# Kernel tuning notes

Hardware: AMD Instinct MI355X
Metric: run time of the kernel (lower is better)

The kernel has to match this reference:

```python
import jax, jax.numpy as jnp
import numpy as np

N_NODES = 100000
N_EDGES = 3200000
IN_F = 128
HEADS = 8
OUT_C = 2  # GATConv out_channels hardcoded to 2 in the source
NEG_SLOPE = 0.2  # PyG GATConv default leaky_relu slope


def setup_inputs() -> dict:
    key = jax.random.key(0)
    ks = jax.random.split(key, 9)
    x = jax.random.normal(ks[0], (N_NODES, IN_F), dtype=jnp.float32)
    edge_index = jax.random.randint(ks[1], (2, N_EDGES), 0, N_NODES, dtype=jnp.int64)
    edge_attr = jax.random.uniform(ks[2], (N_EDGES, 1), dtype=jnp.float32)
    s = 1.0 / np.sqrt(IN_F)
    W = jax.random.normal(ks[3], (IN_F, HEADS * OUT_C), dtype=jnp.float32) * s
    att_src = jax.random.normal(ks[4], (HEADS, OUT_C), dtype=jnp.float32) * 0.5
    att_dst = jax.random.normal(ks[5], (HEADS, OUT_C), dtype=jnp.float32) * 0.5
    bias_gat = jnp.zeros((HEADS * OUT_C,), dtype=jnp.float32)
    W_fc = jax.random.normal(ks[6], (HEADS * OUT_C, 2), dtype=jnp.float32) * 0.25
    b_fc = jnp.zeros((2,), dtype=jnp.float32)
    return {"x": x, "edge_index": edge_index, "edge_attr": edge_attr,
            "W": W, "att_src": att_src, "att_dst": att_dst,
            "bias_gat": bias_gat, "W_fc": W_fc, "b_fc": b_fc}


def reference(x, edge_index, edge_attr, W, att_src, att_dst, bias_gat, W_fc, b_fc):
    # edge_attr is ignored: GATConv was built without edge_dim, matching the source.
    N = x.shape[0]
    # PyG GATConv adds self-loops by default
    loops = jnp.arange(N, dtype=edge_index.dtype)
    src = jnp.concatenate([edge_index[0], loops])  # [E']
    dst = jnp.concatenate([edge_index[1], loops])  # [E']

    h = (x @ W).reshape(N, HEADS, OUT_C)                 # [N,H,C]
    a_src = jnp.einsum('nhc,hc->nh', h, att_src)          # [N,H]
    a_dst = jnp.einsum('nhc,hc->nh', h, att_dst)          # [N,H]

    logits = jax.nn.leaky_relu(a_src[src] + a_dst[dst], negative_slope=NEG_SLOPE)  # [E',H]
    # segment softmax over edges grouped by destination node (self-loops ensure non-empty segments)
    seg_max = jax.ops.segment_max(logits, dst, num_segments=N)   # [N,H]
    p = jnp.exp(logits - seg_max[dst])                            # [E',H]
    seg_sum = jax.ops.segment_sum(p, dst, num_segments=N)         # [N,H]
    alpha = p / seg_sum[dst]                                      # [E',H]

    msg = alpha[:, :, None] * h[src]                              # [E',H,C]
    agg = jax.ops.segment_sum(msg, dst, num_segments=N)           # [N,H,C]
    gat_out = agg.reshape(N, HEADS * OUT_C) + bias_gat            # concat heads + bias
    return gat_out @ W_fc + b_fc                                  # [N,2]
```

## Files before the change

kernel.cpp:

```cpp
#include <hip/hip_runtime.h>
#include <hip/hip_fp16.h>

#define N_NODES 100000
#define IN_F 128
#define NF 16
#define HEADS 8
#define NEG_SLOPE 0.2f
#define LOG2E 1.44269504f

#define RB 128
#define LOG_RB 7
#define NB 782
#define SBITS 17
#define SMASK ((1u << SBITS) - 1)
#define BIN_C 4096
#define CAPB 4672


__device__ __forceinline__ void phase1_body(
    int pb, const float* __restrict__ x, const float* __restrict__ W,
    __half* __restrict__ rec, float* Ws)
{
    int t = threadIdx.x;
    for (int i = t; i < IN_F * NF; i += 512) Ws[i] = W[i];
    __syncthreads();

    int tid  = pb * 512 + t;
    int node = tid >> 4;
    int j    = tid & 15;
    if (node >= N_NODES) return;

    const float4* xr4 = (const float4*)(x + (size_t)node * IN_F);
    float acc = 0.f;
    #pragma unroll 8
    for (int k4 = 0; k4 < IN_F / 4; ++k4) {
        float4 xv = xr4[k4];
        acc = fmaf(xv.x, Ws[(4 * k4 + 0) * NF + j], acc);
        acc = fmaf(xv.y, Ws[(4 * k4 + 1) * NF + j], acc);
        acc = fmaf(xv.z, Ws[(4 * k4 + 2) * NF + j], acc);
        acc = fmaf(xv.w, Ws[(4 * k4 + 3) * NF + j], acc);
    }
    rec[(size_t)node * NF + j] = __float2half(acc);
}

__global__ __launch_bounds__(512) void fused_p1_bin(
    const int* __restrict__ ei, int* __restrict__ bin_cursor,
    unsigned* __restrict__ bins,
    const float* __restrict__ x, const float* __restrict__ W,
    __half* __restrict__ rec, int E, int SB)
{
    __shared__ union {
        struct {
            unsigned staging[BIN_C];
            unsigned short bin16[BIN_C];
            int hist[NB], offs[NB], cur[NB], gbase[NB];
            int wsum[8], woff[8];
        } b;
        float Ws[IN_F * NF];
    } sm;

    int idx = blockIdx.x;
    bool is_bin = (idx % 5 == 0) && (idx / 5 < SB);
    if (!is_bin) {
        int cb = (idx + 4) / 5; if (cb > SB) cb = SB;
        phase1_body(idx - cb, x, W, rec, sm.Ws);
        return;
    }

    int t = threadIdx.x;
    int base = (idx / 5) * BIN_C;
    int n_valid = E - base;
    if (n_valid > BIN_C) n_valid = BIN_C;
    if (n_valid < 0) n_valid = 0;

    int es[8], ed[8];
    #pragma unroll
    for (int k = 0; k < 8; ++k) {
        int i = t + 512 * k;
        bool v = i < n_valid;
        es[k] = v ? ei[base + i] : 0;
        ed[k] = v ? ei[E + base + i] : -1;
    }

    for (int b = t; b < NB; b += 512) sm.b.hist[b] = 0;
    __syncthreads();

    #pragma unroll
    for (int k = 0; k < 8; ++k)
        if (ed[k] >= 0) atomicAdd(&sm.b.hist[ed[k] >> LOG_RB], 1);
    __syncthreads();

    int h2[2], sum = 0;
    #pragma unroll
    for (int k = 0; k < 2; ++k) {
        int b = 2 * t + k;
        h2[k] = (b < NB) ? sm.b.hist[b] : 0;
        sum += h2[k];
    }
    int lane = t & 63, wid = t >> 6;
    int v = sum;
    #pragma unroll
    for (int o = 1; o < 64; o <<= 1) {
        int u = __shfl_up(v, o);
        if (lane >= o) v += u;
    }
    if (lane == 63) sm.b.wsum[wid] = v;
    __syncthreads();
    if (t == 0) { int r = 0; for (int w = 0; w < 8; ++w) { sm.b.woff[w] = r; r += sm.b.wsum[w]; } }
    __syncthreads();
    int run = sm.b.woff[wid] + v - sum;
    #pragma unroll
    for (int k = 0; k < 2; ++k) {
        int b = 2 * t + k;
        if (b < NB) { sm.b.offs[b] = run; sm.b.cur[b] = run; }
        run += h2[k];
    }
    __syncthreads();
    for (int b = t; b < NB; b += 512)
        sm.b.gbase[b] = sm.b.hist[b] ? atomicAdd(&bin_cursor[b], sm.b.hist[b]) : 0;
    __syncthreads();

    #pragma unroll
    for (int k = 0; k < 8; ++k) {
        if (ed[k] >= 0) {
            int b = ed[k] >> LOG_RB;
            int slot = atomicAdd(&sm.b.cur[b], 1);
            sm.b.staging[slot] = ((unsigned)(ed[k] & (RB - 1)) << SBITS) | (unsigned)es[k];
            sm.b.bin16[slot] = (unsigned short)b;
        }
    }
    __syncthreads();

    for (int i = t; i < n_valid; i += 512) {
        int b = sm.b.bin16[i];
        int pos = sm.b.gbase[b] + (i - sm.b.offs[b]);
        if (pos < CAPB) bins[(size_t)b * CAPB + pos] = sm.b.staging[i];
    }
}

__global__ __launch_bounds__(512) void accum4_kernel(
    const unsigned* __restrict__ bins, const int* __restrict__ bin_cursor,
    const __half* __restrict__ rec,
    const float* __restrict__ att_src, const float* __restrict__ att_dst,
    const float* __restrict__ bias, const float* __restrict__ Wfc,
    const float* __restrict__ bfc, float* __restrict__ out)
{
    __shared__ unsigned staging[CAPB];
    __shared__ int hist[RB], offs[RB + 1], cur[RB];

    int t = threadIdx.x;
    int b = blockIdx.x;
    int node0 = b * RB;

    for (int i = t; i < RB; i += 512) hist[i] = 0;
    __syncthreads();

    int cnt = bin_cursor[b];
    if (cnt > CAPB) cnt = CAPB;
    const unsigned* seg = bins + (size_t)b * CAPB;

    unsigned rcache[10];
    int nk = 0;
    for (int i = t; i < cnt; i += 512) rcache[nk++] = seg[i];

    for (int k = 0; k < nk; ++k)
        atomicAdd(&hist[rcache[k] >> SBITS], 1);
    __syncthreads();

    if (t < 64) {
        int h0 = hist[2 * t], h1 = hist[2 * t + 1];
        int v = h0 + h1;
        int inc = v;
        #pragma unroll
        for (int o = 1; o < 64; o <<= 1) {
            int u = __shfl_up(inc, o);
            if (t >= o) inc += u;
        }
        int ex = inc - v;
        offs[2 * t] = ex;          cur[2 * t] = ex;
        offs[2 * t + 1] = ex + h0; cur[2 * t + 1] = ex + h0;
        if (t == 63) offs[RB] = inc;
    }
    __syncthreads();

    for (int k = 0; k < nk; ++k) {
        unsigned r = rcache[k];
        int slot = atomicAdd(&cur[r >> SBITS], 1);
        staging[slot] = r & SMASK;
    }
    __syncthreads();

    int wv = t >> 6, lane = t & 63;
    int h_id = lane & 7, e_off = lane >> 3;

    float as0 = att_src[2 * h_id] * LOG2E, as1 = att_src[2 * h_id + 1] * LOG2E;
    float ad0 = att_dst[2 * h_id] * LOG2E, ad1 = att_dst[2 * h_id + 1] * LOG2E;
    float b0 = bias[2 * h_id], b1 = bias[2 * h_id + 1];
    float w00 = Wfc[(2 * h_id) * 2 + 0],     w01 = Wfc[(2 * h_id) * 2 + 1];
    float w10 = Wfc[(2 * h_id + 1) * 2 + 0], w11 = Wfc[(2 * h_id + 1) * 2 + 1];
    float c0 = bfc[0], c1 = bfc[1];

    for (int k = 0; k < RB / 8; ++k) {
        int dl = wv + 8 * k;
        int n = node0 + dl;
        if (n >= N_NODES) break;
        int st  = offs[dl];
        int deg = offs[dl + 1] - st;

        __half2 hn = *(const __half2*)(rec + (size_t)n * NF + 2 * h_id);
        float hn0 = __half2float(hn.x), hn1 = __half2float(hn.y);
        float adst_h = ad0 * hn0 + ad1 * hn1;

        float den = 0.f, num0 = 0.f, num1 = 0.f;

        for (int i = e_off; i < deg; i += 8) {
            int s = staging[st + i];
            __half2 hs = *(const __half2*)(rec + (size_t)s * NF + 2 * h_id);
            float h0 = __half2float(hs.x), h1 = __half2float(hs.y);
            float l = fmaf(as0, h0, fmaf(as1, h1, adst_h));
            l = l > 0.f ? l : NEG_SLOPE * l;
            float p = exp2f(l);
            den += p;
            num0 = fmaf(p, h0, num0);
            num1 = fmaf(p, h1, num1);
        }
        #pragma unroll
        for (int m = 8; m < 64; m <<= 1) {
            den  += __shfl_xor(den,  m);
            num0 += __shfl_xor(num0, m);
            num1 += __shfl_xor(num1, m);
        }
        {
            float l = fmaf(as0, hn0, fmaf(as1, hn1, adst_h));
            l = l > 0.f ? l : NEG_SLOPE * l;
            float p = exp2f(l);
            den += p;
            num0 = fmaf(p, hn0, num0);
            num1 = fmaf(p, hn1, num1);
        }
        float g0 = num0 / den + b0;
        float g1 = num1 / den + b1;
        float o0 = g0 * w00 + g1 * w10;
        float o1 = g0 * w01 + g1 * w11;
        #pragma unroll
        for (int m = 1; m < 8; m <<= 1) {
            o0 += __shfl_xor(o0, m);
            o1 += __shfl_xor(o1, m);
        }
        if (lane == 0) {
            float2 res = { o0 + c0, o1 + c1 };
            *(float2*)(out + (size_t)n * 2) = res;
        }
    }
}

extern "C" void kernel_launch(void* const* d_in, const int* in_sizes, int n_in,
                              void* d_out, int out_size, void* d_ws, size_t ws_size,
                              hipStream_t stream)
{
    const float* x       = (const float*)d_in[0];
    const int*   ei      = (const int*)d_in[1];
    const float* W       = (const float*)d_in[3];
    const float* att_src = (const float*)d_in[4];
    const float* att_dst = (const float*)d_in[5];
    const float* bias    = (const float*)d_in[6];
    const float* Wfc     = (const float*)d_in[7];
    const float* bfc     = (const float*)d_in[8];
    float*       out     = (float*)d_out;

    const int E  = in_sizes[1] / 2;
    const int SB = (E + BIN_C - 1) / BIN_C;
    const int PB = (N_NODES * 16 + 511) / 512;

    __half* rec        = (__half*)d_ws;
    int*    bin_cursor = (int*)((char*)d_ws + (size_t)N_NODES * NF * 2);
    size_t  bins_off   = (((size_t)((char*)bin_cursor - (char*)d_ws)) + NB * 4 + 4095) & ~(size_t)4095;
    unsigned* bins     = (unsigned*)((char*)d_ws + bins_off);

    hipMemsetAsync(bin_cursor, 0, NB * sizeof(int), stream);

    fused_p1_bin<<<SB + PB, 512, 0, stream>>>(
        ei, bin_cursor, bins, x, W, rec, E, SB);
    accum4_kernel<<<NB, 512, 0, stream>>>(
        bins, bin_cursor, rec, att_src, att_dst, bias, Wfc, bfc, out);
}
```

Measured before the change: 219.0 us.

## Coarsen scatter bins to 256 nodes and split accumulation into two half-blocks

Doubles the destination bin width so the scatter phase handles 391 bins, one per thread, with fewer global cursor atomics and larger contiguous writes. The accumulate kernel now launches two blocks per bin. Each block reads the whole bin but keeps only the edges for its 128-node half. This halves scatter-side bin overhead at the cost of each bin's edge list being read twice in the accumulate phase, plus a larger register cache per thread.

Measured after the change: 217.9 us. No clear change (-0.5%).

```diff
diff --git a/kernel.cpp b/kernel.cpp
--- a/kernel.cpp
+++ b/kernel.cpp
@@ -8,13 +8,14 @@
 #define NEG_SLOPE 0.2f
 #define LOG2E 1.44269504f
 
-#define RB 128
-#define LOG_RB 7
-#define NB 782
+#define RB 256
+#define LOG_RB 8
+#define NB 391
 #define SBITS 17
 #define SMASK ((1u << SBITS) - 1)
 #define BIN_C 4096
-#define CAPB 4672
+#define CAPB 9024
+#define HCAP 4736
 
 
 __device__ __forceinline__ void phase1_body(
@@ -82,7 +83,7 @@
         ed[k] = v ? ei[E + base + i] : -1;
     }
 
-    for (int b = t; b < NB; b += 512) sm.b.hist[b] = 0;
+    if (t < NB) sm.b.hist[t] = 0;
     __syncthreads();
 
     #pragma unroll
@@ -90,13 +91,7 @@
         if (ed[k] >= 0) atomicAdd(&sm.b.hist[ed[k] >> LOG_RB], 1);
     __syncthreads();
 
-    int h2[2], sum = 0;
-    #pragma unroll
-    for (int k = 0; k < 2; ++k) {
-        int b = 2 * t + k;
-        h2[k] = (b < NB) ? sm.b.hist[b] : 0;
-        sum += h2[k];
-    }
+    int sum = (t < NB) ? sm.b.hist[t] : 0;
     int lane = t & 63, wid = t >> 6;
     int v = sum;
     #pragma unroll
@@ -109,15 +104,10 @@
     if (t == 0) { int r = 0; for (int w = 0; w < 8; ++w) { sm.b.woff[w] = r; r += sm.b.wsum[w]; } }
     __syncthreads();
     int run = sm.b.woff[wid] + v - sum;
-    #pragma unroll
-    for (int k = 0; k < 2; ++k) {
-        int b = 2 * t + k;
-        if (b < NB) { sm.b.offs[b] = run; sm.b.cur[b] = run; }
-        run += h2[k];
-    }
-    __syncthreads();
-    for (int b = t; b < NB; b += 512)
-        sm.b.gbase[b] = sm.b.hist[b] ? atomicAdd(&bin_cursor[b], sm.b.hist[b]) : 0;
+    if (t < NB) { sm.b.offs[t] = run; sm.b.cur[t] = run; }
+    __syncthreads();
+    if (t < NB)
+        sm.b.gbase[t] = sm.b.hist[t] ? atomicAdd(&bin_cursor[t], sm.b.hist[t]) : 0;
     __syncthreads();
 
     #pragma unroll
@@ -138,33 +128,36 @@
     }
 }
 
-__global__ __launch_bounds__(512) void accum4_kernel(
+__global__ __launch_bounds__(512) void accum5_kernel(
     const unsigned* __restrict__ bins, const int* __restrict__ bin_cursor,
     const __half* __restrict__ rec,
     const float* __restrict__ att_src, const float* __restrict__ att_dst,
     const float* __restrict__ bias, const float* __restrict__ Wfc,
     const float* __restrict__ bfc, float* __restrict__ out)
 {
-    __shared__ unsigned staging[CAPB];
-    __shared__ int hist[RB], offs[RB + 1], cur[RB];
+    __shared__ unsigned staging[HCAP];
+    __shared__ int hist[128], offs[129], cur[128];
 
     int t = threadIdx.x;
-    int b = blockIdx.x;
-    int node0 = b * RB;
-
-    for (int i = t; i < RB; i += 512) hist[i] = 0;
-    __syncthreads();
-
-    int cnt = bin_cursor[b];
+    int sb   = blockIdx.x >> 1;
+    int half = blockIdx.x & 1;
+    int node0 = sb * RB + half * 128;
+
+    if (t < 128) hist[t] = 0;
+    __syncthreads();
+
+    int cnt = bin_cursor[sb];
     if (cnt > CAPB) cnt = CAPB;
-    const unsigned* seg = bins + (size_t)b * CAPB;
-
-    unsigned rcache[10];
+    const unsigned* seg = bins + (size_t)sb * CAPB;
+
+    unsigned rcache[18];
     int nk = 0;
     for (int i = t; i < cnt; i += 512) rcache[nk++] = seg[i];
 
-    for (int k = 0; k < nk; ++k)
-        atomicAdd(&hist[rcache[k] >> SBITS], 1);
+    for (int k = 0; k < nk; ++k) {
+        int dl = rcache[k] >> SBITS;
+        if ((dl >> 7) == half) atomicAdd(&hist[dl & 127], 1);
+    }
     __syncthreads();
 
     if (t < 64) {
@@ -179,14 +172,17 @@
         int ex = inc - v;
         offs[2 * t] = ex;          cur[2 * t] = ex;
         offs[2 * t + 1] = ex + h0; cur[2 * t + 1] = ex + h0;
-        if (t == 63) offs[RB] = inc;
+        if (t == 63) offs[128] = inc;
     }
     __syncthreads();
 
     for (int k = 0; k < nk; ++k) {
         unsigned r = rcache[k];
-        int slot = atomicAdd(&cur[r >> SBITS], 1);
-        staging[slot] = r & SMASK;
+        int dl = r >> SBITS;
+        if ((dl >> 7) == half) {
+            int slot = atomicAdd(&cur[dl & 127], 1);
+            if (slot < HCAP) staging[slot] = r & SMASK;
+        }
     }
     __syncthreads();
 
@@ -200,12 +196,15 @@
     float w10 = Wfc[(2 * h_id + 1) * 2 + 0], w11 = Wfc[(2 * h_id + 1) * 2 + 1];
     float c0 = bfc[0], c1 = bfc[1];
 
-    for (int k = 0; k < RB / 8; ++k) {
-        int dl = wv + 8 * k;
-        int n = node0 + dl;
+    for (int k = 0; k < 16; ++k) {
+        int ln = wv + 8 * k;
+        int n = node0 + ln;
         if (n >= N_NODES) break;
-        int st  = offs[dl];
-        int deg = offs[dl + 1] - st;
+        int st  = offs[ln];
+        int end = offs[ln + 1];
+        if (st > HCAP) st = HCAP;
+        if (end > HCAP) end = HCAP;
+        int deg = end - st;
 
         __half2 hn = *(const __half2*)(rec + (size_t)n * NF + 2 * h_id);
         float hn0 = __half2float(hn.x), hn1 = __half2float(hn.y);
@@ -281,6 +280,6 @@
 
     fused_p1_bin<<<SB + PB, 512, 0, stream>>>(
         ei, bin_cursor, bins, x, W, rec, E, SB);
-    accum4_kernel<<<NB, 512, 0, stream>>>(
+    accum5_kernel<<<2 * NB, 512, 0, stream>>>(
         bins, bin_cursor, rec, att_src, att_dst, bias, Wfc, bfc, out);
 }
```
